# Optimization experiments

Hardware: AMD Instinct MI355X
Metric: run time of the kernel (lower is better)

The kernel has to match this reference:

```python
import jax, jax.numpy as jnp
import numpy as np

B, S, D = 2, 2048, 2048
H, KVH = 32, 8
HD = D // H          # 64
Q_OUT = H * HD       # 2048
KV_OUT = KVH * HD    # 512
THETA = 10000.0


def setup_inputs() -> dict:
    key = jax.random.key(0)
    k1, k2, k3 = jax.random.split(key, 3)
    x = jax.random.normal(k1, (B, S, D), dtype=jnp.float32)
    w_qkv = jax.random.normal(k2, (Q_OUT + 2 * KV_OUT, D), dtype=jnp.float32) * 0.02
    w_out = jax.random.normal(k3, (D, D), dtype=jnp.float32) * 0.02
    gain = jnp.ones((1,), dtype=jnp.float32)
    return {"x": x, "w_qkv": w_qkv, "w_out": w_out, "gain": gain}


def _rope(t):
    # t: [b, s, h, hd]; non-interleaved (half-split) RoPE, positions = arange(s)
    s, hd = t.shape[1], t.shape[-1]
    inv_freq = 1.0 / (THETA ** (jnp.arange(0, hd // 2, dtype=jnp.float32) * 2.0 / hd))
    ang = jnp.arange(s, dtype=jnp.float32)[:, None] * inv_freq[None, :]  # [s, hd/2]
    cos = jnp.cos(ang)[None, :, None, :]
    sin = jnp.sin(ang)[None, :, None, :]
    t1, t2 = t[..., : hd // 2], t[..., hd // 2 :]
    return jnp.concatenate([t1 * cos - t2 * sin, t2 * cos + t1 * sin], axis=-1)


def _rmsnorm(t, eps=1e-6):
    # per-head-dim RMS normalization in fp32 (QK-norm)
    inv = jax.lax.rsqrt(jnp.mean(t * t, axis=-1, keepdims=True) + eps)
    return t * inv


def reference(x, w_qkv, w_out, gain):
    proj = jnp.einsum("bsd,od->bso", x, w_qkv)
    Q = proj[..., :Q_OUT].reshape(B, S, H, HD)
    K = proj[..., Q_OUT : Q_OUT + KV_OUT].reshape(B, S, KVH, HD)
    V = proj[..., Q_OUT + KV_OUT :].reshape(B, S, KVH, HD)

    Q = _rope(Q)
    K = _rope(K)

    # GQA: repeat_interleave kv heads to match query heads
    rep = H // KVH
    K = jnp.repeat(K, rep, axis=2)  # [b, s, H, hd]
    V = jnp.repeat(V, rep, axis=2)

    # value residual path (disabled): alpha1=1, alpha2=0, scale=1 -> V * rsqrt(1 + 1e-8)
    V = V * jax.lax.rsqrt(jnp.float32(1.0 + 1e-8))

    # QK-RMSNorm with learnable scalar gain on q
    Qn = _rmsnorm(Q) * gain
    Kn = _rmsnorm(K)

    scale = 1.0 / jnp.sqrt(jnp.float32(HD))
    scores = jnp.einsum("bqhd,bkhd->bhqk", Qn, Kn) * scale  # [b, H, S, S]
    causal = jnp.tril(jnp.ones((S, S), dtype=bool))
    scores = jnp.where(causal[None, None], scores, jnp.float32(-1e30))
    p = jax.nn.softmax(scores, axis=-1)
    attn = jnp.einsum("bhqk,bkhd->bqhd", p, V)  # [b, S, H, hd]

    # rearrange '(h b) seq hd -> b seq (h hd)': head index is outer in feature dim
    attn_cat = attn.transpose(0, 1, 2, 3).reshape(B, S, H * HD)
    attn_out = jnp.einsum("bsd,od->bso", attn_cat, w_out)

    # module returns (attn_out, V) with V in (h*b, seq, hd) layout
    V_flat = V.transpose(2, 0, 1, 3).reshape(H * B, S, HD)
    return attn_out, V_flat
```

## Files before the change

### kernel.cpp

```cpp
#include <hip/hip_runtime.h>
#include <hip/hip_bf16.h>
#include <cstdint>
#include <cstddef>

#define B_ 2
#define S_ 2048
#define D_ 2048
#define H_ 32
#define KVH_ 8
#define HD_ 64
#define PROJN 3072

typedef unsigned short u16;
typedef unsigned int u32;
typedef __attribute__((ext_vector_type(8))) short short8;
typedef __attribute__((ext_vector_type(4))) short short4v;
typedef __attribute__((ext_vector_type(4))) float f32x4;

__device__ __forceinline__ u16 f2bf(float f) {
  __hip_bfloat16 h = __float2bfloat16(f);
  return *reinterpret_cast<u16*>(&h);
}

__device__ __forceinline__ float fast_exp2(float x) {
  float r;
  asm("v_exp_f32 %0, %1" : "=v"(r) : "v"(x));
  return r;
}

__device__ __forceinline__ u32 pack2bf(float lo, float hi) {
  u32 a = __float_as_uint(lo) + 0x8000u;
  u32 b = __float_as_uint(hi) + 0x8000u;
  return __builtin_amdgcn_perm(b, a, 0x07060302);
}

#define GLDS16(g, l)                                                           \
  __builtin_amdgcn_global_load_lds(                                            \
      (const __attribute__((address_space(1))) void*)(g),                      \
      (__attribute__((address_space(3))) void*)(l), 16, 0, 0)

__global__ __launch_bounds__(256) void pack3(const float* __restrict__ x,
                                             const float* __restrict__ wqkv,
                                             const float* __restrict__ wout,
                                             u16* __restrict__ xb,
                                             u16* __restrict__ wqkvb,
                                             u16* __restrict__ woutb) {
  const int bid = blockIdx.x;
  const float* in;
  u16* out;
  int base;
  if (bid < 4096) { in = x; out = xb; base = bid; }
  else if (bid < 7168) { in = wqkv; out = wqkvb; base = bid - 4096; }
  else { in = wout; out = woutb; base = bid - 7168; }
  const int i = (base * 256 + threadIdx.x) * 8;
  const float4* p = reinterpret_cast<const float4*>(in + i);
  float4 a = p[0], b = p[1];
  union { short8 v; u16 u[8]; } r;
  r.u[0] = f2bf(a.x); r.u[1] = f2bf(a.y); r.u[2] = f2bf(a.z); r.u[3] = f2bf(a.w);
  r.u[4] = f2bf(b.x); r.u[5] = f2bf(b.y); r.u[6] = f2bf(b.z); r.u[7] = f2bf(b.w);
  *reinterpret_cast<short8*>(out + i) = r.v;
}

__global__ __launch_bounds__(256) void rope_tabT(float* __restrict__ tct,
                                                 float* __restrict__ tst) {
  int i = blockIdx.x * 256 + threadIdx.x;
  int j = i >> 11, s = i & 2047;
  float e = (float)(2 * j) / 64.0f;
  float inv_freq = 1.0f / powf(10000.0f, e);
  float ang = (float)s * inv_freq;
  tct[i] = cosf(ang);
  tst[i] = sinf(ang);
}

__global__ __launch_bounds__(512) void gemm_bt(const u16* __restrict__ A,
                                               const u16* __restrict__ Bw,
                                               float* __restrict__ C, int M,
                                               int N, int K) {
  __shared__ u16 As[2][128 * 64];
  __shared__ u16 Bs[2][128 * 64];
  const int tid = threadIdx.x;
  const int lane = tid & 63;
  const int wave = tid >> 6;
  const int ntile = N >> 7;
  const int m0 = (blockIdx.x / ntile) << 7;
  const int n0 = (blockIdx.x % ntile) << 7;
  const int wr = (wave >> 1) << 5;
  const int wc = (wave & 1) << 6;
  const int arow = lane & 15;
  const int kgrp = lane >> 4;

  const f32x4 zero4 = {0.f, 0.f, 0.f, 0.f};
  f32x4 acc[2][4];
#pragma unroll
  for (int m = 0; m < 2; m++)
#pragma unroll
    for (int n = 0; n < 4; n++) acc[m][n] = zero4;

  int srow[2], sslot[2];
#pragma unroll
  for (int i = 0; i < 2; i++) {
    int c = i * 512 + tid;
    srow[i] = c >> 3;
    sslot[i] = (c & 7) ^ (srow[i] & 7);
  }

  auto stage = [&](int kt, int buf) {
    const int k0 = kt << 6;
#pragma unroll
    for (int i = 0; i < 2; i++) {
      const u16* ga = A + (size_t)(m0 + srow[i]) * K + k0 + sslot[i] * 8;
      GLDS16(ga, As[buf] + (i * 512 + tid) * 8);
    }
#pragma unroll
    for (int i = 0; i < 2; i++) {
      const u16* gb = Bw + (size_t)(n0 + srow[i]) * K + k0 + sslot[i] * 8;
      GLDS16(gb, Bs[buf] + (i * 512 + tid) * 8);
    }
  };

  const int KT = K >> 6;
  stage(0, 0);
  stage(1, 1);
  int cur = 0;
  for (int kt = 0; kt < KT; kt++) {
    if (kt + 1 < KT) asm volatile("s_waitcnt vmcnt(4)" ::: "memory");
    else             asm volatile("s_waitcnt vmcnt(0)" ::: "memory");
    __builtin_amdgcn_s_barrier();
    __builtin_amdgcn_sched_barrier(0);
    const u16* Asb = As[cur];
    const u16* Bsb = Bs[cur];
#pragma unroll
    for (int ks = 0; ks < 2; ks++) {
      const int sd = ks * 4 + kgrp;
      short8 a[2], b[4];
#pragma unroll
      for (int m = 0; m < 2; m++) {
        int r = wr + m * 16 + arow;
        a[m] = *reinterpret_cast<const short8*>(Asb + r * 64 + ((sd ^ (r & 7)) << 3));
      }
#pragma unroll
      for (int n = 0; n < 4; n++) {
        int r = wc + n * 16 + arow;
        b[n] = *reinterpret_cast<const short8*>(Bsb + r * 64 + ((sd ^ (r & 7)) << 3));
      }
#pragma unroll
      for (int m = 0; m < 2; m++)
#pragma unroll
        for (int n = 0; n < 4; n++)
          acc[m][n] = __builtin_amdgcn_mfma_f32_16x16x32_bf16(a[m], b[n], acc[m][n], 0, 0, 0);
    }
    __builtin_amdgcn_sched_barrier(0);
    __builtin_amdgcn_s_barrier();
    if (kt + 2 < KT) stage(kt + 2, cur);
    cur ^= 1;
  }

  const int crow = kgrp * 4;
#pragma unroll
  for (int m = 0; m < 2; m++) {
#pragma unroll
    for (int n = 0; n < 4; n++) {
      float* cp = C + (size_t)(m0 + wr + m * 16 + crow) * N + n0 + wc + n * 16 + arow;
#pragma unroll
      for (int r = 0; r < 4; r++) cp[(size_t)r * N] = acc[m][n][r];
    }
  }
}

__global__ __launch_bounds__(512) void gemm_qkv(
    const u16* __restrict__ A, const u16* __restrict__ Bw,
    const float* __restrict__ tct, const float* __restrict__ tst,
    const float* __restrict__ gain, float* __restrict__ projV,
    u16* __restrict__ Qn, u16* __restrict__ Kn) {
  __shared__ u16 As[2][128 * 64];
  __shared__ u16 Bs[2][128 * 64];
  const int tid = threadIdx.x;
  const int lane = tid & 63;
  const int wave = tid >> 6;
  const int ntile = PROJN >> 7;
  const int m0 = (blockIdx.x / ntile) << 7;
  const int n0 = (blockIdx.x % ntile) << 7;
  const int wr = (wave >> 1) << 5;
  const int wc = (wave & 1) << 6;
  const int ql = lane & 15;
  const int g = lane >> 4;
  const int K = 2048;

  const f32x4 zero4 = {0.f, 0.f, 0.f, 0.f};
  f32x4 acc[2][4];
#pragma unroll
  for (int m = 0; m < 2; m++)
#pragma unroll
    for (int n = 0; n < 4; n++) acc[m][n] = zero4;

  int srow[2], sslot[2];
#pragma unroll
  for (int i = 0; i < 2; i++) {
    int c = i * 512 + tid;
    srow[i] = c >> 3;
    sslot[i] = (c & 7) ^ (srow[i] & 7);
  }

  auto stage = [&](int kt, int buf) {
    const int k0 = kt << 6;
#pragma unroll
    for (int i = 0; i < 2; i++) {
      const u16* ga = A + (size_t)(m0 + srow[i]) * K + k0 + sslot[i] * 8;
      GLDS16(ga, As[buf] + (i * 512 + tid) * 8);
    }
#pragma unroll
    for (int i = 0; i < 2; i++) {
      const u16* gb = Bw + (size_t)(n0 + srow[i]) * K + k0 + sslot[i] * 8;
      GLDS16(gb, Bs[buf] + (i * 512 + tid) * 8);
    }
  };

  const int KT = 32;
  stage(0, 0);
  stage(1, 1);
  int cur = 0;
  for (int kt = 0; kt < KT; kt++) {
    if (kt + 1 < KT) asm volatile("s_waitcnt vmcnt(4)" ::: "memory");
    else             asm volatile("s_waitcnt vmcnt(0)" ::: "memory");
    __builtin_amdgcn_s_barrier();
    __builtin_amdgcn_sched_barrier(0);
    const u16* Asb = As[cur];
    const u16* Bsb = Bs[cur];
#pragma unroll
    for (int ks = 0; ks < 2; ks++) {
      const int sd = ks * 4 + g;
      short8 a[2], b[4];
#pragma unroll
      for (int m = 0; m < 2; m++) {
        int r = wr + m * 16 + ql;
        a[m] = *reinterpret_cast<const short8*>(Asb + r * 64 + ((sd ^ (r & 7)) << 3));
      }
#pragma unroll
      for (int n = 0; n < 4; n++) {
        int r = wc + n * 16 + ql;
        b[n] = *reinterpret_cast<const short8*>(Bsb + r * 64 + ((sd ^ (r & 7)) << 3));
      }
#pragma unroll
      for (int m = 0; m < 2; m++)
#pragma unroll
        for (int n = 0; n < 4; n++)
          acc[m][n] = __builtin_amdgcn_mfma_f32_16x16x32_bf16(a[m], b[n], acc[m][n], 0, 0, 0);
    }
    __builtin_amdgcn_sched_barrier(0);
    __builtin_amdgcn_s_barrier();
    if (kt + 2 < KT) stage(kt + 2, cur);
    cur ^= 1;
  }

  const int hslice = (n0 + wc) >> 6;
  const int browbase = m0 + wr + 4 * g;
  const int bb = (m0 + wr) >> 11;

  if (hslice >= 40) {
    float* dstV = projV + (size_t)browbase * 512 + (hslice - 40) * 64;
#pragma unroll
    for (int m = 0; m < 2; m++)
#pragma unroll
      for (int n = 0; n < 4; n++) {
        float* dp = dstV + (size_t)(16 * m) * 512 + n * 16 + ql;
#pragma unroll
        for (int r = 0; r < 4; r++) dp[(size_t)r * 512] = acc[m][n][r];
      }
    return;
  }

  const bool isQ = (hslice < 32);
  const float scale = isQ ? gain[0] * 0.18033688011112042f : 1.0f;
  u16* outp = isQ ? Qn + ((size_t)(bb * H_ + hslice)) * S_ * HD_
                  : Kn + ((size_t)(bb * KVH_ + (hslice - 32))) * S_ * HD_;
  const int jj0 = ql, jj1 = 16 + ql;

#pragma unroll
  for (int m = 0; m < 2; m++) {
    const int sb = (browbase + 16 * m) & (S_ - 1);
    float c0a[4], c1a[4], s0a[4], s1a[4];
    *reinterpret_cast<float4*>(c0a) = *reinterpret_cast<const float4*>(&tct[jj0 * 2048 + sb]);
    *reinterpret_cast<float4*>(c1a) = *reinterpret_cast<const float4*>(&tct[jj1 * 2048 + sb]);
    *reinterpret_cast<float4*>(s0a) = *reinterpret_cast<const float4*>(&tst[jj0 * 2048 + sb]);
    *reinterpret_cast<float4*>(s1a) = *reinterpret_cast<const float4*>(&tst[jj1 * 2048 + sb]);
    float o[4][4], iv[4];
#pragma unroll
    for (int r = 0; r < 4; r++) {
      const float a0 = acc[m][0][r], a1 = acc[m][1][r];
      const float a2 = acc[m][2][r], a3 = acc[m][3][r];
      const float l0 = a0 * c0a[r] - a2 * s0a[r];
      const float l1 = a1 * c1a[r] - a3 * s1a[r];
      const float h0 = a2 * c0a[r] + a0 * s0a[r];
      const float h1 = a3 * c1a[r] + a1 * s1a[r];
      o[0][r] = l0; o[1][r] = l1; o[2][r] = h0; o[3][r] = h1;
      float sr = (l0 * l0 + l1 * l1) + (h0 * h0 + h1 * h1);
      sr += __shfl_xor(sr, 1);
      sr += __shfl_xor(sr, 2);
      sr += __shfl_xor(sr, 4);
      sr += __shfl_xor(sr, 8);
      iv[r] = rsqrtf(sr * (1.0f / 64.0f) + 1e-6f) * scale;
    }
#pragma unroll
    for (int n = 0; n < 4; n++) {
      const int d = n * 16 + ql;
#pragma unroll
      for (int r = 0; r < 4; r++)
        outp[(size_t)(sb + r) * HD_ + d] = f2bf(o[n][r] * iv[r]);
    }
  }
}

__global__ __launch_bounds__(256) void vtrans(const float* __restrict__ projV,
                                              u16* __restrict__ Vt,
                                              float* __restrict__ Vout) {
  __shared__ float tile[64][65];
  const int bid = blockIdx.x;
  const int st = bid & 31;
  const int s0 = st << 6;
  const int kvh = (bid >> 5) & 7;
  const int b = bid >> 8;
  const int t = threadIdx.x;
  const int sr = t >> 2;
  const int d0 = (t & 3) << 4;
  const float* src = projV + ((size_t)(b * S_ + s0 + sr)) * 512 + kvh * 64 + d0;
  float v[16];
#pragma unroll
  for (int i = 0; i < 16; i += 4) {
    float4 x = *reinterpret_cast<const float4*>(src + i);
    v[i] = x.x; v[i + 1] = x.y; v[i + 2] = x.z; v[i + 3] = x.w;
  }
#pragma unroll
  for (int hh = 0; hh < 4; hh++) {
    int hq = kvh * 4 + hh;
    float* dst = Vout + (((size_t)(hq * B_ + b)) * S_ + s0 + sr) * HD_ + d0;
#pragma unroll
    for (int i = 0; i < 16; i += 4)
      *reinterpret_cast<float4*>(dst + i) = make_float4(v[i], v[i + 1], v[i + 2], v[i + 3]);
  }
#pragma unroll
  for (int i = 0; i < 16; i++) tile[sr][d0 + i] = v[i];
  __syncthreads();
  const int d = t >> 2;
  const int sc = (t & 3) << 4;
  union { short8 v8; u16 u[8]; } o0, o1;
#pragma unroll
  for (int i = 0; i < 8; i++) o0.u[i] = f2bf(tile[sc + i][d]);
#pragma unroll
  for (int i = 0; i < 8; i++) o1.u[i] = f2bf(tile[sc + 8 + i][d]);
  u16* dst = Vt + (((size_t)(b * KVH_ + kvh)) * HD_ + d) * S_ + s0 + sc;
  *reinterpret_cast<short8*>(dst) = o0.v8;
  *reinterpret_cast<short8*>(dst + 8) = o1.v8;
}

__global__ __launch_bounds__(256, 2) void attn_fwd(const u16* __restrict__ Qn,
                                                   const u16* __restrict__ Kn,
                                                   const u16* __restrict__ Vt,
                                                   u16* __restrict__ Aout) {
  __shared__ u16 Ks[2][64 * 64];
  __shared__ u16 Vs[2][64 * 64];
  __shared__ u16 Ps[4][1024];
  const int bid = blockIdx.x;
  const int grp = bid & 15;
  const int i = bid >> 4;
  const int qt = 63 - i;
  const int b = grp >> 3;
  const int kvh = grp & 7;
  const int q0 = qt << 5;
  const int JT = (qt >> 1) + 1;
  const int tid = threadIdx.x;
  const int lane = tid & 63;
  const int wave = tid >> 6;
  const int h = kvh * 4 + wave;
  const int ql = lane & 15;
  const int g = lane >> 4;

  short8 qa[2][2];
  int rowq[2];
#pragma unroll
  for (int f = 0; f < 2; f++) {
    rowq[f] = q0 + 16 * f + ql;
    const u16* qb = Qn + (((size_t)(b * H_ + h)) * S_ + rowq[f]) * HD_;
    qa[f][0] = *reinterpret_cast<const short8*>(qb + g * 8);
    qa[f][1] = *reinterpret_cast<const short8*>(qb + 32 + g * 8);
  }

  const f32x4 zero4 = {0.f, 0.f, 0.f, 0.f};
  f32x4 oacc[4][2];
#pragma unroll
  for (int dn = 0; dn < 4; dn++)
#pragma unroll
    for (int f = 0; f < 2; f++) oacc[dn][f] = zero4;
  float psum[2] = {0.f, 0.f};

  const u16* kg = Kn + ((size_t)(b * KVH_ + kvh)) * S_ * HD_;
  const u16* vg = Vt + ((size_t)(b * KVH_ + kvh)) * HD_ * S_;

  const int c0 = tid, c1 = 256 + tid;
  const int r0 = c0 >> 3, sl0 = (c0 & 7) ^ (r0 & 7);
  const int r1 = c1 >> 3, sl1 = (c1 & 7) ^ (r1 & 7);
  const int xsw2 = (ql & 7) << 2;

  auto stage = [&](int jt, int buf) {
    const int j0 = jt << 6;
    GLDS16(kg + (size_t)(j0 + r0) * HD_ + sl0 * 8, Ks[buf] + c0 * 8);
    GLDS16(kg + (size_t)(j0 + r1) * HD_ + sl1 * 8, Ks[buf] + c1 * 8);
    GLDS16(vg + (size_t)r0 * S_ + j0 + sl0 * 8, Vs[buf] + c0 * 8);
    GLDS16(vg + (size_t)r1 * S_ + j0 + sl1 * 8, Vs[buf] + c1 * 8);
  };

  stage(0, 0);
  __syncthreads();
  int cur = 0;
  for (int jt = 0; jt < JT; jt++) {
    if (jt + 1 < JT) stage(jt + 1, cur ^ 1);
    const int j0 = jt << 6;
    const u16* ksb = Ks[cur];
    const u16* vsb = Vs[cur];
    const bool diag = (jt == JT - 1);

    f32x4 sc[4][2];
#pragma unroll
    for (int n = 0; n < 4; n++)
#pragma unroll
      for (int f = 0; f < 2; f++) sc[n][f] = zero4;
    __builtin_amdgcn_s_setprio(1);
#pragma unroll
    for (int ks = 0; ks < 2; ks++) {
      const int sd = ks * 4 + g;
#pragma unroll
      for (int n = 0; n < 4; n++) {
        const int r = n * 16 + ql;
        short8 kf = *reinterpret_cast<const short8*>(ksb + r * 64 + ((sd ^ (r & 7)) << 3));
        sc[n][0] = __builtin_amdgcn_mfma_f32_16x16x32_bf16(kf, qa[0][ks], sc[n][0], 0, 0, 0);
        sc[n][1] = __builtin_amdgcn_mfma_f32_16x16x32_bf16(kf, qa[1][ks], sc[n][1], 0, 0, 0);
      }
    }
    __builtin_amdgcn_s_setprio(0);

    short8 pa[2][2];
#pragma unroll
    for (int f = 0; f < 2; f++) {
      float pv[4][4];
#pragma unroll
      for (int n = 0; n < 4; n++)
#pragma unroll
        for (int r = 0; r < 4; r++)
          pv[n][r] = fast_exp2(sc[n][f][r]);
      if (diag) {
#pragma unroll
        for (int n = 0; n < 4; n++)
#pragma unroll
          for (int r = 0; r < 4; r++)
            if ((j0 + n * 16 + 4 * g + r) > rowq[f]) pv[n][r] = 0.f;
      }
      u32* pw32 = reinterpret_cast<u32*>(Ps[wave]);
#pragma unroll
      for (int n = 0; n < 4; n++) {
        psum[f] += (pv[n][0] + pv[n][1]) + (pv[n][2] + pv[n][3]);
        const int idx = ql * 32 + (((n << 3) + (g << 1)) ^ xsw2);
        pw32[idx] = pack2bf(pv[n][0], pv[n][1]);
        pw32[idx + 1] = pack2bf(pv[n][2], pv[n][3]);
      }
#pragma unroll
      for (int ks = 0; ks < 2; ks++)
        pa[f][ks] = *reinterpret_cast<const short8*>(
            Ps[wave] + ql * 64 + ((32 * ks + 8 * g) ^ (xsw2 << 1)));
    }

    __builtin_amdgcn_s_setprio(1);
#pragma unroll
    for (int ks = 0; ks < 2; ks++) {
      const int sd = ks * 4 + g;
#pragma unroll
      for (int dn = 0; dn < 4; dn++) {
        const int vr = dn * 16 + ql;
        short8 vf = *reinterpret_cast<const short8*>(vsb + vr * 64 + ((sd ^ (vr & 7)) << 3));
        oacc[dn][0] = __builtin_amdgcn_mfma_f32_16x16x32_bf16(vf, pa[0][ks], oacc[dn][0], 0, 0, 0);
        oacc[dn][1] = __builtin_amdgcn_mfma_f32_16x16x32_bf16(vf, pa[1][ks], oacc[dn][1], 0, 0, 0);
      }
    }
    __builtin_amdgcn_s_setprio(0);

    __syncthreads();
    cur ^= 1;
  }

#pragma unroll
  for (int f = 0; f < 2; f++) {
    float s = psum[f];
    s += __shfl_xor(s, 16);
    s += __shfl_xor(s, 32);
    const float il = 1.0f / s;
#pragma unroll
    for (int dn = 0; dn < 4; dn++) {
      union { short4v v; u16 uu[4]; } o;
#pragma unroll
      for (int r = 0; r < 4; r++) o.uu[r] = f2bf(oacc[dn][f][r] * il);
      u16* dst = Aout + ((size_t)b * S_ + rowq[f]) * D_ + h * HD_ + dn * 16 + 4 * g;
      *reinterpret_cast<short4v*>(dst) = o.v;
    }
  }
}

extern "C" void kernel_launch(void* const* d_in, const int* in_sizes, int n_in,
                              void* d_out, int out_size, void* d_ws,
                              size_t ws_size, hipStream_t stream) {
  const float* x = (const float*)d_in[0];
  const float* wqkv = (const float*)d_in[1];
  const float* wout = (const float*)d_in[2];
  const float* gain = (const float*)d_in[3];

  float* out_attn = (float*)d_out;
  float* out_vflat = out_attn + (size_t)B_ * S_ * D_;

  uint8_t* w = (uint8_t*)d_ws;
  u16* xb      = (u16*)(w);
  u16* wqkvb   = (u16*)(w + 16777216);
  u16* woutb   = (u16*)(w + 29360128);
  float* projV = (float*)(w + 37748736);
  u16* Qn      = (u16*)(w + 46137344);
  u16* Kn      = (u16*)(w + 62914560);
  u16* Vt      = (u16*)(w + 67108864);
  u16* attnb   = (u16*)(w + 71303168);
  float* tct   = (float*)(w + 88080384);
  float* tst   = (float*)(w + 88342528);

  pack3<<<9216, 256, 0, stream>>>(x, wqkv, wout, xb, wqkvb, woutb);
  rope_tabT<<<256, 256, 0, stream>>>(tct, tst);

  gemm_qkv<<<(4096 / 128) * (3072 / 128), 512, 0, stream>>>(
      xb, wqkvb, tct, tst, gain, projV, Qn, Kn);
  vtrans<<<B_ * KVH_ * (S_ / 64), 256, 0, stream>>>(projV, Vt, out_vflat);
  attn_fwd<<<B_ * KVH_ * (S_ / 32), 256, 0, stream>>>(Qn, Kn, Vt, attnb);
  gemm_bt<<<(4096 / 128) * (2048 / 128), 512, 0, stream>>>(attnb, woutb,
                                                           out_attn, 4096,
                                                           2048, 2048);
}
```

Before: 201.2 us.

## Enlarge QKV GEMM M-tile to 256 and drop LDS double buffering

The QKV projection GEMM tile grows from 128x128 to 256x128, so each wave computes a 64x64 sub-tile with a 4x4 accumulator array, and the grid shrinks to half as many blocks. The double-buffered LDS pipeline with explicit vmcnt waits is replaced by a single buffer with __syncthreads before and after each stage. The aim is more data reuse per block, higher MFMA density per LDS load and fewer blocks. The cost is losing the overlap between global loads and compute, higher register pressure from 64 accumulators, and only 384 blocks to spread across the GPU's compute units.

```diff
diff --git a/kernel.cpp b/kernel.cpp
--- a/kernel.cpp
+++ b/kernel.cpp
@@ -172,84 +172,75 @@
     const float* __restrict__ tct, const float* __restrict__ tst,
     const float* __restrict__ gain, float* __restrict__ projV,
     u16* __restrict__ Qn, u16* __restrict__ Kn) {
-  __shared__ u16 As[2][128 * 64];
-  __shared__ u16 Bs[2][128 * 64];
+  __shared__ u16 As[256 * 64];
+  __shared__ u16 Bs[128 * 64];
   const int tid = threadIdx.x;
   const int lane = tid & 63;
   const int wave = tid >> 6;
   const int ntile = PROJN >> 7;
-  const int m0 = (blockIdx.x / ntile) << 7;
+  const int m0 = (blockIdx.x / ntile) << 8;
   const int n0 = (blockIdx.x % ntile) << 7;
-  const int wr = (wave >> 1) << 5;
+  const int wr = (wave >> 1) << 6;
   const int wc = (wave & 1) << 6;
   const int ql = lane & 15;
   const int g = lane >> 4;
   const int K = 2048;
 
   const f32x4 zero4 = {0.f, 0.f, 0.f, 0.f};
-  f32x4 acc[2][4];
-#pragma unroll
-  for (int m = 0; m < 2; m++)
+  f32x4 acc[4][4];
+#pragma unroll
+  for (int m = 0; m < 4; m++)
 #pragma unroll
     for (int n = 0; n < 4; n++) acc[m][n] = zero4;
 
-  int srow[2], sslot[2];
-#pragma unroll
-  for (int i = 0; i < 2; i++) {
-    int c = i * 512 + tid;
+  int srow[6], sslot[6];
+#pragma unroll
+  for (int i = 0; i < 6; i++) {
+    int c = (i < 4 ? i * 512 + tid : (i - 4) * 512 + tid);
     srow[i] = c >> 3;
     sslot[i] = (c & 7) ^ (srow[i] & 7);
   }
 
-  auto stage = [&](int kt, int buf) {
+  auto stage = [&](int kt) {
     const int k0 = kt << 6;
 #pragma unroll
-    for (int i = 0; i < 2; i++) {
+    for (int i = 0; i < 4; i++) {
       const u16* ga = A + (size_t)(m0 + srow[i]) * K + k0 + sslot[i] * 8;
-      GLDS16(ga, As[buf] + (i * 512 + tid) * 8);
-    }
-#pragma unroll
-    for (int i = 0; i < 2; i++) {
+      GLDS16(ga, As + (i * 512 + tid) * 8);
+    }
+#pragma unroll
+    for (int i = 4; i < 6; i++) {
       const u16* gb = Bw + (size_t)(n0 + srow[i]) * K + k0 + sslot[i] * 8;
-      GLDS16(gb, Bs[buf] + (i * 512 + tid) * 8);
+      GLDS16(gb, Bs + ((i - 4) * 512 + tid) * 8);
     }
   };
 
-  const int KT = 32;
-  stage(0, 0);
-  stage(1, 1);
-  int cur = 0;
-  for (int kt = 0; kt < KT; kt++) {
-    if (kt + 1 < KT) asm volatile("s_waitcnt vmcnt(4)" ::: "memory");
-    else             asm volatile("s_waitcnt vmcnt(0)" ::: "memory");
-    __builtin_amdgcn_s_barrier();
-    __builtin_amdgcn_sched_barrier(0);
-    const u16* Asb = As[cur];
-    const u16* Bsb = Bs[cur];
+  stage(0);
+  for (int kt = 0;; kt++) {
+    __syncthreads();
 #pragma unroll
     for (int ks = 0; ks < 2; ks++) {
       const int sd = ks * 4 + g;
-      short8 a[2], b[4];
-#pragma unroll
-      for (int m = 0; m < 2; m++) {
+      short8 a[4], b[4];
+#pragma unroll
+      for (int m = 0; m < 4; m++) {
         int r = wr + m * 16 + ql;
-        a[m] = *reinterpret_cast<const short8*>(Asb + r * 64 + ((sd ^ (r & 7)) << 3));
+        a[m] = *reinterpret_cast<const short8*>(As + r * 64 + ((sd ^ (r & 7)) << 3));
       }
 #pragma unroll
       for (int n = 0; n < 4; n++) {
         int r = wc + n * 16 + ql;
-        b[n] = *reinterpret_cast<const short8*>(Bsb + r * 64 + ((sd ^ (r & 7)) << 3));
-      }
-#pragma unroll
-      for (int m = 0; m < 2; m++)
+        b[n] = *reinterpret_cast<const short8*>(Bs + r * 64 + ((sd ^ (r & 7)) << 3));
+      }
+#pragma unroll
+      for (int m = 0; m < 4; m++)
 #pragma unroll
         for (int n = 0; n < 4; n++)
           acc[m][n] = __builtin_amdgcn_mfma_f32_16x16x32_bf16(a[m], b[n], acc[m][n], 0, 0, 0);
     }
-    __builtin_amdgcn_sched_barrier(0);
-    __builtin_amdgcn_s_barrier();
-    if (kt + 2 < KT) stage(kt + 2, cur);
-    cur ^= 1;
+    if (kt + 1 == 32) break;
+    __syncthreads();
+    stage(kt + 1);
   }
 
   const int hslice = (n0 + wc) >> 6;
@@ -259,7 +250,7 @@
   if (hslice >= 40) {
     float* dstV = projV + (size_t)browbase * 512 + (hslice - 40) * 64;
 #pragma unroll
-    for (int m = 0; m < 2; m++)
+    for (int m = 0; m < 4; m++)
 #pragma unroll
       for (int n = 0; n < 4; n++) {
         float* dp = dstV + (size_t)(16 * m) * 512 + n * 16 + ql;
@@ -276,7 +267,7 @@
   const int jj0 = ql, jj1 = 16 + ql;
 
 #pragma unroll
-  for (int m = 0; m < 2; m++) {
+  for (int m = 0; m < 4; m++) {
     const int sb = (browbase + 16 * m) & (S_ - 1);
     float c0a[4], c1a[4], s0a[4], s1a[4];
     *reinterpret_cast<float4*>(c0a) = *reinterpret_cast<const float4*>(&tct[jj0 * 2048 + sb]);
@@ -528,7 +519,7 @@
   pack3<<<9216, 256, 0, stream>>>(x, wqkv, wout, xb, wqkvb, woutb);
   rope_tabT<<<256, 256, 0, stream>>>(tct, tst);
 
-  gemm_qkv<<<(4096 / 128) * (3072 / 128), 512, 0, stream>>>(
+  gemm_qkv<<<(4096 / 256) * (3072 / 128), 512, 0, stream>>>(
       xb, wqkvb, tct, tst, gain, projV, Qn, Kn);
   vtrans<<<B_ * KVH_ * (S_ / 64), 256, 0, stream>>>(projV, Vt, out_vflat);
   attn_fwd<<<B_ * KVH_ * (S_ / 32), 256, 0, stream>>>(Qn, Kn, Vt, attnb);
```

After: 224.9 us. 11.7% more time.
